# Kernel tuning notes

Hardware: AMD Instinct MI355X
Metric: run time of the kernel (lower is better)

Reference implementation:

```python
import jax, jax.numpy as jnp
import numpy as np

T, B, DIN, H, AA, L = 1024, 32, 256, 256, 21, 2


def setup_inputs() -> dict:
    key = jax.random.key(0)
    ks = jax.random.split(key, 8)
    scale = 0.05

    def rn(i, shape):
        return jax.random.normal(ks[i], shape, dtype=jnp.float32) * scale

    return {
        "x": jax.random.normal(ks[0], (B, T, DIN), dtype=jnp.float32),
        "hidden": jnp.zeros((2 * L, B, H), jnp.float32),  # accepted but unused, as in torch forward
        # layer 0: input DIN -> per-direction 4 chunks of H; layer 1: input 2H
        "w_l0": rn(1, (DIN, 2, 4, H)),
        "wc_l0": rn(2, (2, 2, H)),            # [dir, (v_f, v_r), H]
        "b_l0": jnp.zeros((2, 2, H), jnp.float32),  # [dir, (b_f, b_r), H]
        "w_l1": rn(3, (2 * H, 2, 4, H)),
        "wc_l1": rn(4, (2, 2, H)),
        "b_l1": jnp.zeros((2, 2, H), jnp.float32),
        "fc1_w": rn(5, (H, 2 * H)),
        "fc1_b": jnp.zeros((H,), jnp.float32),
        "lp_w": rn(6, (AA, H)),
        "lp_b": jnp.zeros((AA,), jnp.float32),
    }


def _sru_scan(u, vf, vr, bf, br):
    # u: (T, B, 4, H) with chunks [candidate, forget, reset, highway]
    def step(c, ut):
        f = jax.nn.sigmoid(ut[:, 1] + vf * c + bf)
        c2 = f * c + (1.0 - f) * ut[:, 0]
        r = jax.nn.sigmoid(ut[:, 2] + vr * c + br)
        h = r * c2 + (1.0 - r) * ut[:, 3]
        return c2, h

    c0 = jnp.zeros((u.shape[1], u.shape[-1]), u.dtype)
    _, hs = jax.lax.scan(step, c0, u)
    return hs  # (T, B, H)


def _sru_layer(x, w, wc, b):
    # x: (T, B, Din); w: (Din, 2, 4, H)
    U = jnp.einsum('tbd,dnkh->tbnkh', x, w)
    hf = _sru_scan(U[:, :, 0], wc[0, 0], wc[0, 1], b[0, 0], b[0, 1])
    hb = _sru_scan(U[::-1, :, 1], wc[1, 0], wc[1, 1], b[1, 0], b[1, 1])[::-1]
    return jnp.concatenate([hf, hb], axis=-1)  # (T, B, 2H)


def reference(x, hidden, w_l0, wc_l0, b_l0, w_l1, wc_l1, b_l1, fc1_w, fc1_b, lp_w, lp_b):
    h = jnp.transpose(x, (1, 0, 2))  # (T, B, DIN)
    h = _sru_layer(h, w_l0, wc_l0, b_l0)
    h = _sru_layer(h, w_l1, wc_l1, b_l1)
    h = jnp.transpose(h, (1, 0, 2))  # (B, T, 2H)
    h = h @ fc1_w.T + fc1_b
    logits = h @ lp_w.T + lp_b
    return jax.nn.log_softmax(logits, axis=-1)  # (B, T, AA)
```

## Files before the change

kernel.cpp:

```cpp
#include <hip/hip_runtime.h>
#include <hip/hip_bf16.h>

#define T_DIM 1024
#define B_DIM 32
#define DIN_DIM 256
#define H_DIM 256
#define AA_DIM 21
#define M_ROWS (B_DIM * T_DIM)

typedef __attribute__((ext_vector_type(8))) short bf16x8;
typedef __attribute__((ext_vector_type(4))) float f32x4;

typedef __attribute__((address_space(3))) void lds_void;
typedef const __attribute__((address_space(1))) void glb_void;

#define LOG2E_F 1.44269504088896340736f

__device__ __forceinline__ void gload_lds16(const void* g, void* l) {
    __builtin_amdgcn_global_load_lds((glb_void*)g, (lds_void*)l, 16, 0, 0);
}

__device__ __forceinline__ float b2f(unsigned short v) {
    unsigned u = ((unsigned)v) << 16;
    float f;
    __builtin_memcpy(&f, &u, 4);
    return f;
}

__device__ __forceinline__ unsigned short f2bu(float f) {
    __hip_bfloat16 h = __float2bfloat16(f);
    unsigned short u;
    __builtin_memcpy(&u, &h, 2);
    return u;
}

#define CVT_V0 2097152
#define CVT_N1 524288
#define CVT_N2 1048576
#define CVT_V3 32768
#define CVT_N4 8192
#define CVT_TOT (CVT_V0 + CVT_N1 + CVT_N2 + CVT_V3 + CVT_N4)
__global__ __launch_bounds__(256) void cvt_all(
    const float* __restrict__ x,  const float* __restrict__ w0,
    const float* __restrict__ w1, const float* __restrict__ fcw,
    const float* __restrict__ lpw,
    __hip_bfloat16* __restrict__ xb,  __hip_bfloat16* __restrict__ w0t,
    __hip_bfloat16* __restrict__ w1t, __hip_bfloat16* __restrict__ fcwb,
    __hip_bfloat16* __restrict__ lpwb)
{
    int i = blockIdx.x * 256 + threadIdx.x;
    if (i < CVT_V0) {
        float4 v = ((const float4*)x)[i];
        ushort4 o = { f2bu(v.x), f2bu(v.y), f2bu(v.z), f2bu(v.w) };
        ((ushort4*)xb)[i] = o;
        return;
    }
    i -= CVT_V0;
    if (i < CVT_N1) {
        int kk = i >> 11, rem = i & 2047;
        int dir = rem >> 10, k = (rem >> 8) & 3, h = rem & 255;
        w0t[(long)(dir * 1024 + h * 4 + k) * 256 + kk] = __float2bfloat16(w0[i]);
        return;
    }
    i -= CVT_N1;
    if (i < CVT_N2) {
        int kk = i >> 11, rem = i & 2047;
        int dir = rem >> 10, k = (rem >> 8) & 3, h = rem & 255;
        w1t[(long)(dir * 1024 + h * 4 + k) * 512 + kk] = __float2bfloat16(w1[i]);
        return;
    }
    i -= CVT_N2;
    if (i < CVT_V3) {
        float4 v = ((const float4*)fcw)[i];
        ushort4 o = { f2bu(v.x), f2bu(v.y), f2bu(v.z), f2bu(v.w) };
        ((ushort4*)fcwb)[i] = o;
        return;
    }
    i -= CVT_V3;
    if (i < CVT_N4) {
        int n = i >> 8, k = i & 255;
        lpwb[i] = __float2bfloat16(n < AA_DIM ? lpw[n * 256 + k] : 0.0f);
    }
}

__device__ __forceinline__ void stage_tile256(
    const __hip_bfloat16* __restrict__ A,
    const __hip_bfloat16* __restrict__ Bt,
    char* buf, long m0, long n0, int K, int kb,
    int wave, int ldrow, int gkoff)
{
#pragma unroll
    for (int i = 0; i < 4; ++i) {
        const int cid = wave * 4 + i;
        const int rc  = cid >> 1;
        const int kh  = cid & 1;
        const long row = rc * 16 + ldrow;
        const int koff = kb + kh * 32 + gkoff;
        gload_lds16(A  + (m0 + row) * (long)K + koff,
                    buf + rc * 2048 + kh * 1024);
        gload_lds16(Bt + (n0 + row) * (long)K + koff,
                    buf + 32768 + rc * 2048 + kh * 1024);
    }
}

#define MFMA16(d, a, b) d = __builtin_amdgcn_mfma_f32_16x16x32_bf16(a, b, d, 0, 0, 0)

__global__ __launch_bounds__(512, 2) void gemm256_u2(
    const __hip_bfloat16* __restrict__ A,
    const __hip_bfloat16* __restrict__ Bt,
    __hip_bfloat16* __restrict__ C,
    int K, int nbShift)
{
    __shared__ __align__(16) char smb[131072];

    const int tid  = threadIdx.x;
    const int lane = tid & 63;
    const int wave = tid >> 6;
    const int wm   = wave >> 2;
    const int wn   = wave & 3;

    const int L  = blockIdx.x;
    const int s  = L >> 3;
    const int nb = s & ((1 << nbShift) - 1);
    const int mb = ((s >> nbShift) << 3) + (L & 7);
    const long n0 = (long)nb * 256;
    const long m0 = (long)mb * 256;

    const int ldrow = lane >> 2;
    const int ldq   = lane & 3;
    const int gq    = ldq ^ ((ldrow >> 1) & 3);
    const int gkoff = gq * 8;

    const int fr = lane & 15;
    const int kq = lane >> 4;
    const int sw = (kq ^ ((fr >> 1) & 3)) * 16;

    f32x4 acc[8][4] = {};
    const int NT = K >> 6;

    stage_tile256(A, Bt, smb,         m0, n0, K, 0,  wave, ldrow, gkoff);
    __builtin_amdgcn_sched_barrier(0);
    stage_tile256(A, Bt, smb + 65536, m0, n0, K, 64, wave, ldrow, gkoff);
    asm volatile("s_waitcnt vmcnt(8)" ::: "memory");
    __builtin_amdgcn_s_barrier();

    for (int kt = 0; kt < NT; ++kt) {
        char* rb = smb + (kt & 1) * 65536;
        const char* Ab = rb + (wm * 8) * 2048;
        const char* Bb = rb + 32768 + (wn * 4) * 2048;
        bf16x8 a0[4], a1[4], bv[4];

#pragma unroll
        for (int i = 0; i < 4; ++i) {
            a0[i] = *(const bf16x8*)(Ab + i * 2048 + fr * 64 + sw);
            bv[i] = *(const bf16x8*)(Bb + i * 2048 + fr * 64 + sw);
        }
        __builtin_amdgcn_s_barrier();
        __builtin_amdgcn_s_setprio(1);
#pragma unroll
        for (int i = 0; i < 4; ++i)
#pragma unroll
            for (int j = 0; j < 4; ++j)
                MFMA16(acc[i][j], a0[i], bv[j]);
        __builtin_amdgcn_s_setprio(0);
        __builtin_amdgcn_s_barrier();

#pragma unroll
        for (int i = 0; i < 4; ++i)
            a1[i] = *(const bf16x8*)(Ab + (4 + i) * 2048 + fr * 64 + sw);
        __builtin_amdgcn_s_barrier();
        __builtin_amdgcn_s_setprio(1);
#pragma unroll
        for (int i = 0; i < 4; ++i)
#pragma unroll
            for (int j = 0; j < 4; ++j)
                MFMA16(acc[4 + i][j], a1[i], bv[j]);
        __builtin_amdgcn_s_setprio(0);
        __builtin_amdgcn_s_barrier();

#pragma unroll
        for (int i = 0; i < 4; ++i) {
            a0[i] = *(const bf16x8*)(Ab + i * 2048 + 1024 + fr * 64 + sw);
            bv[i] = *(const bf16x8*)(Bb + i * 2048 + 1024 + fr * 64 + sw);
        }
        __builtin_amdgcn_s_barrier();
        __builtin_amdgcn_s_setprio(1);
#pragma unroll
        for (int i = 0; i < 4; ++i)
#pragma unroll
            for (int j = 0; j < 4; ++j)
                MFMA16(acc[i][j], a0[i], bv[j]);
        __builtin_amdgcn_s_setprio(0);
        __builtin_amdgcn_s_barrier();

#pragma unroll
        for (int i = 0; i < 4; ++i)
            a1[i] = *(const bf16x8*)(Ab + (4 + i) * 2048 + 1024 + fr * 64 + sw);
        __builtin_amdgcn_s_barrier();
        __builtin_amdgcn_s_setprio(1);
#pragma unroll
        for (int i = 0; i < 4; ++i)
#pragma unroll
            for (int j = 0; j < 4; ++j)
                MFMA16(acc[4 + i][j], a1[i], bv[j]);
        __builtin_amdgcn_s_setprio(0);
        __builtin_amdgcn_s_barrier();

        __builtin_amdgcn_sched_barrier(0);
        if (kt + 2 < NT) {
            stage_tile256(A, Bt, rb, m0, n0, K, (kt + 2) * 64,
                          wave, ldrow, gkoff);
            asm volatile("s_waitcnt vmcnt(8)" ::: "memory");
        } else if (kt + 1 < NT) {
            asm volatile("s_waitcnt vmcnt(0)" ::: "memory");
        }
        __builtin_amdgcn_s_barrier();
    }

    const int col_l = lane & 15;
    const int row_l = (lane >> 4) * 4;
    __hip_bfloat16* smC = (__hip_bfloat16*)smb;
    const int chunk = tid & 31;
    const int rbase = tid >> 5;
#pragma unroll
    for (int p = 0; p < 2; ++p) {
        __syncthreads();
        if (wm == p) {
#pragma unroll
            for (int i = 0; i < 8; ++i)
#pragma unroll
                for (int j = 0; j < 4; ++j)
#pragma unroll
                    for (int r = 0; r < 4; ++r)
                        smC[(i * 16 + row_l + r) * 264 + wn * 64 + j * 16 + col_l] =
                            __float2bfloat16(acc[i][j][r]);
        }
        __syncthreads();
#pragma unroll
        for (int it = 0; it < 8; ++it) {
            const int rr = it * 16 + rbase;
            bf16x8 v = *(const bf16x8*)(smC + rr * 264 + chunk * 8);
            const long gr  = m0 + p * 128 + rr;
            const long gc0 = n0 + chunk * 8;
            const int bI  = (int)(gr >> 10);
            const int t   = (int)(gr & 1023);
            const int dir = (int)(gc0 >> 10);
            const int hg  = ((int)gc0 >> 8) & 3;
            const int beta = bI * 8 + dir * 4 + hg;
            const long base = ((long)beta * 1024 + t) * 256 + ((int)gc0 & 255);
            *(bf16x8*)(C + base) = v;
        }
    }
}

template<int U2OUT>
__global__ __launch_bounds__(256) void gemm_bf16(
    const __hip_bfloat16* __restrict__ A,
    const __hip_bfloat16* __restrict__ Bt,
    const float* __restrict__ bias,
    __hip_bfloat16* __restrict__ C,
    int M, int N, int K, int nbShift)
{
    __shared__ __align__(16) char smb[32768];

    const int tid  = threadIdx.x;
    const int lane = tid & 63;
    const int wave = tid >> 6;
    const int wm = wave & 1;
    const int wn = wave >> 1;

    const int L   = blockIdx.x;
    const int s   = L >> 3;
    const int nb  = s & ((1 << nbShift) - 1);
    const int mb  = ((s >> nbShift) << 3) + (L & 7);
    const long n0 = (long)nb * 128;
    const long m0 = (long)mb * 128;

    f32x4 acc[4][4] = {};

    const int ldrow = lane >> 2;
    const int ldq   = lane & 3;
    const int gq    = ldq ^ ((ldrow >> 1) & 3);
    const int gkoff = gq * 8;

    const int fr = lane & 15;
    const int kq = lane >> 4;
    const int sw = (kq ^ ((fr >> 1) & 3)) * 16;

    for (int kb = 0; kb < K; kb += 64) {
        __syncthreads();
#pragma unroll
        for (int i = 0; i < 4; ++i) {
            const int cid = wave * 4 + i;
            const int rc  = cid >> 1;
            const int kh  = cid & 1;
            const long row = rc * 16 + ldrow;
            const int koff = kb + kh * 32 + gkoff;
            gload_lds16(A  + (m0 + row) * (long)K + koff,
                        smb + rc * 2048 + kh * 1024);
            gload_lds16(Bt + (n0 + row) * (long)K + koff,
                        smb + 16384 + rc * 2048 + kh * 1024);
        }
        __syncthreads();

#pragma unroll
        for (int ss = 0; ss < 2; ++ss) {
            bf16x8 af[4], bfv[4];
#pragma unroll
            for (int i = 0; i < 4; ++i) {
                af[i]  = *(const bf16x8*)(smb + (wm * 4 + i) * 2048 + ss * 1024 + fr * 64 + sw);
                bfv[i] = *(const bf16x8*)(smb + 16384 + (wn * 4 + i) * 2048 + ss * 1024 + fr * 64 + sw);
            }
#pragma unroll
            for (int i = 0; i < 4; ++i)
#pragma unroll
                for (int j = 0; j < 4; ++j)
                    acc[i][j] = __builtin_amdgcn_mfma_f32_16x16x32_bf16(
                        af[i], bfv[j], acc[i][j], 0, 0, 0);
        }
    }

    const int col_l = lane & 15;
    const int row_l = (lane >> 4) * 4;
    __hip_bfloat16* smC = (__hip_bfloat16*)smb;
#pragma unroll
    for (int p = 0; p < 2; ++p) {
        __syncthreads();
        if (wm == p) {
#pragma unroll
            for (int j = 0; j < 4; ++j) {
                const long gc = n0 + wn * 64 + j * 16 + col_l;
                const float bv = bias ? bias[gc] : 0.0f;
#pragma unroll
                for (int i = 0; i < 4; ++i)
#pragma unroll
                    for (int r = 0; r < 4; ++r)
                        smC[(i * 16 + row_l + r) * 132 + wn * 64 + j * 16 + col_l] =
                            __float2bfloat16(acc[i][j][r] + bv);
            }
        }
        __syncthreads();
        const int cb = (tid & 7) * 16;
#pragma unroll
        for (int s2 = 0; s2 < 2; ++s2) {
            const int rr = s2 * 32 + (tid >> 3);
            const long gr = m0 + p * 64 + rr;
            bf16x8 v0 = *(const bf16x8*)(smC + rr * 132 + cb);
            bf16x8 v1 = *(const bf16x8*)(smC + rr * 132 + cb + 8);
            if (U2OUT) {
                const int bI  = (int)(gr >> 10);
                const int t   = (int)(gr & 1023);
                const long gc0 = n0 + cb;
                const int dir = (int)(gc0 >> 10);
                const int hg  = ((int)gc0 >> 8) & 3;
                const int beta = bI * 8 + dir * 4 + hg;
                const long base = ((long)beta * 1024 + t) * 256 + (gc0 & 255);
                *(bf16x8*)(C + base)     = v0;
                *(bf16x8*)(C + base + 8) = v1;
            } else {
                *(bf16x8*)(C + gr * (long)N + n0 + cb)     = v0;
                *(bf16x8*)(C + gr * (long)N + n0 + cb + 8) = v1;
            }
        }
    }
}

#define SCAN_S 64
#define SCAN_NB (T_DIM / SCAN_S)
#define GRP 16

__device__ __forceinline__ float scan_step(
    uint2 u, float c, float nvf, float nvr, float nbf, float nbr,
    __hip_bfloat16* hq)
{
    float u0, u1, u2, u3;
    unsigned a0 = u.x << 16, a1 = u.x & 0xffff0000u;
    unsigned a2 = u.y << 16, a3 = u.y & 0xffff0000u;
    __builtin_memcpy(&u0, &a0, 4); __builtin_memcpy(&u1, &a1, 4);
    __builtin_memcpy(&u2, &a2, 4); __builtin_memcpy(&u3, &a3, 4);
    const float nf0 = __builtin_fmaf(-LOG2E_F, u1, nbf);
    const float nr0 = __builtin_fmaf(-LOG2E_F, u2, nbr);
    const float ef = __builtin_amdgcn_exp2f(__builtin_fmaf(nvf, c, nf0));
    const float er = __builtin_amdgcn_exp2f(__builtin_fmaf(nvr, c, nr0));
    const float f  = __builtin_amdgcn_rcpf(1.0f + ef);
    const float r  = __builtin_amdgcn_rcpf(1.0f + er);
    const float c2 = __builtin_fmaf(f, c - u0, u0);
    const float hv = __builtin_fmaf(r, c2 - u3, u3);
    *hq = __float2bfloat16(hv);
    return c2;
}

__global__ __launch_bounds__(256) void sru_scan(
    const __hip_bfloat16* __restrict__ U2,
    const float* __restrict__ wc,
    const float* __restrict__ bias,
    __hip_bfloat16* __restrict__ hout)
{
    __shared__ __align__(16) char lds[2 * SCAN_S * 512];
    const int tid  = threadIdx.x;
    const int wave = tid >> 6;
    const int lane = tid & 63;
    const int beta = blockIdx.x;
    const int b    = beta >> 3;
    const int dir  = (beta >> 2) & 1;
    const int hg   = beta & 3;
    const int h    = hg * 64 + lane;

    const char* gslice = (const char*)U2 + (size_t)beta * (1024 * 512);

    const float nvf = -LOG2E_F * wc[(dir * 2 + 0) * H_DIM + h];
    const float nvr = -LOG2E_F * wc[(dir * 2 + 1) * H_DIM + h];
    const float nbf = -LOG2E_F * bias[(dir * 2 + 0) * H_DIM + h];
    const float nbr = -LOG2E_F * bias[(dir * 2 + 1) * H_DIM + h];
    __hip_bfloat16* hp = hout + ((long)(b * 1024 + (dir ? 1023 : 0))) * 512 + dir * 256 + h;
    const long hstep = dir ? -512L : 512L;
    float c = 0.0f;

    const int plane = lane & 31;

    if (wave > 0) {
        for (int p = wave - 1; p < SCAN_S / 2; p += 3) {
            const int sl = 2 * p + (lane >> 5);
            const int t  = dir ? (1023 - sl) : sl;
            gload_lds16(gslice + (size_t)t * 512 + plane * 16, lds + p * 1024);
        }
    }
    __syncthreads();

    for (int bat = 0; bat < SCAN_NB; ++bat) {
        if (wave > 0) {
            if (bat + 1 < SCAN_NB) {
                char* halfN = lds + ((bat + 1) & 1) * (SCAN_S * 512);
                const int tb = (bat + 1) * SCAN_S;
                for (int p = wave - 1; p < SCAN_S / 2; p += 3) {
                    const int sl = tb + 2 * p + (lane >> 5);
                    const int t  = dir ? (1023 - sl) : sl;
                    gload_lds16(gslice + (size_t)t * 512 + plane * 16,
                                halfN + p * 1024);
                }
            }
        } else {
            const char* half = lds + (bat & 1) * (SCAN_S * 512);
            __hip_bfloat16* hq = hp + (long)(bat * SCAN_S) * hstep;
            uint2 qa[GRP], qb[GRP];
#pragma unroll
            for (int j = 0; j < GRP; ++j)
                qa[j] = *(const uint2*)(half + (0 * GRP + j) * 512 + (lane << 3));
#pragma unroll
            for (int j = 0; j < GRP; ++j)
                qb[j] = *(const uint2*)(half + (1 * GRP + j) * 512 + (lane << 3));
#pragma unroll
            for (int j = 0; j < GRP; ++j)
                c = scan_step(qa[j], c, nvf, nvr, nbf, nbr, hq + (long)j * hstep);
#pragma unroll
            for (int j = 0; j < GRP; ++j)
                qa[j] = *(const uint2*)(half + (2 * GRP + j) * 512 + (lane << 3));
#pragma unroll
            for (int j = 0; j < GRP; ++j)
                c = scan_step(qb[j], c, nvf, nvr, nbf, nbr, hq + (long)(GRP + j) * hstep);
#pragma unroll
            for (int j = 0; j < GRP; ++j)
                qb[j] = *(const uint2*)(half + (3 * GRP + j) * 512 + (lane << 3));
#pragma unroll
            for (int j = 0; j < GRP; ++j)
                c = scan_step(qa[j], c, nvf, nvr, nbf, nbr, hq + (long)(2 * GRP + j) * hstep);
#pragma unroll
            for (int j = 0; j < GRP; ++j)
                c = scan_step(qb[j], c, nvf, nvr, nbf, nbr, hq + (long)(3 * GRP + j) * hstep);
        }
        __syncthreads();
    }
}

__global__ __launch_bounds__(256) void logits_mfma(
    const __hip_bfloat16* __restrict__ fc,
    const __hip_bfloat16* __restrict__ lpwb,
    const float* __restrict__ lpb,
    float* __restrict__ out)
{
    __shared__ __align__(16) char smb[25088];
    const int tid  = threadIdx.x;
    const int lane = tid & 63;
    const int wave = tid >> 6;
    const long m0  = (long)blockIdx.x * 128;

    for (int idx = tid; idx < 32 * 32; idx += 256) {
        const int rw = idx >> 5, sl = idx & 31;
        *(bf16x8*)(smb + rw * 528 + sl * 16) =
            *(const bf16x8*)(lpwb + rw * 256 + sl * 8);
    }

    const int ldrow = lane >> 2;
    const int ldq   = lane & 3;
    const int gq    = ldq ^ ((ldrow >> 1) & 3);
    const int gkoff = gq * 8;

    const int fr = lane & 15;
    const int kq = lane >> 4;
    const int sw = (kq ^ ((fr >> 1) & 3)) * 16;

    f32x4 acc[2][2] = {};
    for (int kc = 0; kc < 8; ++kc) {
        __syncthreads();
#pragma unroll
        for (int i = 0; i < 2; ++i) {
            const int rc = wave * 2 + i;
            gload_lds16(fc + (m0 + rc * 16 + ldrow) * 256 + kc * 32 + gkoff,
                        smb + 16896 + rc * 1024);
        }
        __syncthreads();
        bf16x8 af[2], bfv[2];
#pragma unroll
        for (int i = 0; i < 2; ++i)
            af[i] = *(const bf16x8*)(smb + 16896 + (wave * 2 + i) * 1024 + fr * 64 + sw);
#pragma unroll
        for (int j = 0; j < 2; ++j)
            bfv[j] = *(const bf16x8*)(smb + (j * 16 + fr) * 528 + kc * 64 + kq * 16);
#pragma unroll
        for (int i = 0; i < 2; ++i)
#pragma unroll
            for (int j = 0; j < 2; ++j)
                acc[i][j] = __builtin_amdgcn_mfma_f32_16x16x32_bf16(
                    af[i], bfv[j], acc[i][j], 0, 0, 0);
    }

    __syncthreads();
    float* smC = (float*)smb;
    const int col_l = lane & 15;
    const int row_l = (lane >> 4) * 4;
#pragma unroll
    for (int j = 0; j < 2; ++j) {
        const int gc = j * 16 + col_l;
        const float bv = (gc < AA_DIM) ? lpb[gc] : 0.0f;
#pragma unroll
        for (int i = 0; i < 2; ++i)
#pragma unroll
            for (int r = 0; r < 4; ++r)
                smC[(wave * 32 + i * 16 + row_l + r) * 36 + gc] = acc[i][j][r] + bv;
    }
    __syncthreads();
    if (tid < 128) {
        const float* rowp = smC + tid * 36;
        float m = rowp[0];
#pragma unroll
        for (int a = 1; a < AA_DIM; ++a) m = fmaxf(m, rowp[a]);
        float s = 0.0f;
#pragma unroll
        for (int a = 0; a < AA_DIM; ++a) s += __expf(rowp[a] - m);
        const float lse = __logf(s) + m;
        float* op = out + (m0 + tid) * AA_DIM;
#pragma unroll
        for (int a = 0; a < AA_DIM; ++a) op[a] = rowp[a] - lse;
    }
}

extern "C" void kernel_launch(void* const* d_in, const int* in_sizes, int n_in,
                              void* d_out, int out_size, void* d_ws, size_t ws_size,
                              hipStream_t stream)
{
    const float* x     = (const float*)d_in[0];
    const float* w_l0  = (const float*)d_in[2];
    const float* wc_l0 = (const float*)d_in[3];
    const float* b_l0  = (const float*)d_in[4];
    const float* w_l1  = (const float*)d_in[5];
    const float* wc_l1 = (const float*)d_in[6];
    const float* b_l1  = (const float*)d_in[7];
    const float* fc1_w = (const float*)d_in[8];
    const float* fc1_b = (const float*)d_in[9];
    const float* lp_w  = (const float*)d_in[10];
    const float* lp_b  = (const float*)d_in[11];
    float* out = (float*)d_out;

    char* ws = (char*)d_ws;
    __hip_bfloat16* U      = (__hip_bfloat16*)(ws);
    __hip_bfloat16* h0b    = (__hip_bfloat16*)(ws + 134217728);
    __hip_bfloat16* h1b    = (__hip_bfloat16*)(ws + 167772160);
    __hip_bfloat16* xb     = (__hip_bfloat16*)(ws + 201326592);
    __hip_bfloat16* fcob   = xb;
    __hip_bfloat16* w0t    = (__hip_bfloat16*)(ws + 218103808);
    __hip_bfloat16* w1t    = (__hip_bfloat16*)(ws + 219152384);
    __hip_bfloat16* fc1wb  = (__hip_bfloat16*)(ws + 221249536);
    __hip_bfloat16* lpwb   = (__hip_bfloat16*)(ws + 221511680);

    cvt_all<<<(CVT_TOT + 255) / 256, 256, 0, stream>>>(
        x, w_l0, w_l1, fc1_w, lp_w, xb, w0t, w1t, fc1wb, lpwb);

    gemm256_u2<<<1024, 512, 0, stream>>>(xb, w0t, U, DIN_DIM, 3);
    sru_scan<<<256, 256, 0, stream>>>(U, wc_l0, b_l0, h0b);
    gemm256_u2<<<1024, 512, 0, stream>>>(h0b, w1t, U, 512, 3);
    sru_scan<<<256, 256, 0, stream>>>(U, wc_l1, b_l1, h1b);
    gemm_bf16<0><<<512, 256, 0, stream>>>(
        h1b, fc1wb, fc1_b, fcob, M_ROWS, 256, 512, 1);
    logits_mfma<<<M_ROWS / 128, 256, 0, stream>>>(fcob, lpwb, lp_b, out);
}
```

Measured before the change: 389.1 us.

## Fuse fc1 GEMM with logits projection and log-softmax in one kernel

Replaces the separate fc1 GEMM and logits kernels with one fused kernel. Each 512-thread block computes a 128x256 fc1 tile with double-buffered LDS staging, keeps the bf16 result in LDS, and then runs the 21-class projection and log-softmax on it. This removes the global write and re-read of the fc1 intermediate and one kernel launch. In exchange, only 256 blocks at one block per CU run, each loading the full N=256 weight slice, so latency hiding may suffer.

```diff
diff --git a/kernel.cpp b/kernel.cpp
--- a/kernel.cpp
+++ b/kernel.cpp
@@ -18,13 +18,6 @@
 
 __device__ __forceinline__ void gload_lds16(const void* g, void* l) {
     __builtin_amdgcn_global_load_lds((glb_void*)g, (lds_void*)l, 16, 0, 0);
-}
-
-__device__ __forceinline__ float b2f(unsigned short v) {
-    unsigned u = ((unsigned)v) << 16;
-    float f;
-    __builtin_memcpy(&f, &u, 4);
-    return f;
 }
 
 __device__ __forceinline__ unsigned short f2bu(float f) {
@@ -83,6 +76,8 @@
     }
 }
 
+#define MFMA16(d, a, b) d = __builtin_amdgcn_mfma_f32_16x16x32_bf16(a, b, d, 0, 0, 0)
+
 __device__ __forceinline__ void stage_tile256(
     const __hip_bfloat16* __restrict__ A,
     const __hip_bfloat16* __restrict__ Bt,
@@ -102,8 +97,6 @@
                     buf + 32768 + rc * 2048 + kh * 1024);
     }
 }
-
-#define MFMA16(d, a, b) d = __builtin_amdgcn_mfma_f32_16x16x32_bf16(a, b, d, 0, 0, 0)
 
 __global__ __launch_bounds__(512, 2) void gemm256_u2(
     const __hip_bfloat16* __restrict__ A,
@@ -249,118 +242,6 @@
             const int beta = bI * 8 + dir * 4 + hg;
             const long base = ((long)beta * 1024 + t) * 256 + ((int)gc0 & 255);
             *(bf16x8*)(C + base) = v;
-        }
-    }
-}
-
-template<int U2OUT>
-__global__ __launch_bounds__(256) void gemm_bf16(
-    const __hip_bfloat16* __restrict__ A,
-    const __hip_bfloat16* __restrict__ Bt,
-    const float* __restrict__ bias,
-    __hip_bfloat16* __restrict__ C,
-    int M, int N, int K, int nbShift)
-{
-    __shared__ __align__(16) char smb[32768];
-
-    const int tid  = threadIdx.x;
-    const int lane = tid & 63;
-    const int wave = tid >> 6;
-    const int wm = wave & 1;
-    const int wn = wave >> 1;
-
-    const int L   = blockIdx.x;
-    const int s   = L >> 3;
-    const int nb  = s & ((1 << nbShift) - 1);
-    const int mb  = ((s >> nbShift) << 3) + (L & 7);
-    const long n0 = (long)nb * 128;
-    const long m0 = (long)mb * 128;
-
-    f32x4 acc[4][4] = {};
-
-    const int ldrow = lane >> 2;
-    const int ldq   = lane & 3;
-    const int gq    = ldq ^ ((ldrow >> 1) & 3);
-    const int gkoff = gq * 8;
-
-    const int fr = lane & 15;
-    const int kq = lane >> 4;
-    const int sw = (kq ^ ((fr >> 1) & 3)) * 16;
-
-    for (int kb = 0; kb < K; kb += 64) {
-        __syncthreads();
-#pragma unroll
-        for (int i = 0; i < 4; ++i) {
-            const int cid = wave * 4 + i;
-            const int rc  = cid >> 1;
-            const int kh  = cid & 1;
-            const long row = rc * 16 + ldrow;
-            const int koff = kb + kh * 32 + gkoff;
-            gload_lds16(A  + (m0 + row) * (long)K + koff,
-                        smb + rc * 2048 + kh * 1024);
-            gload_lds16(Bt + (n0 + row) * (long)K + koff,
-                        smb + 16384 + rc * 2048 + kh * 1024);
-        }
-        __syncthreads();
-
-#pragma unroll
-        for (int ss = 0; ss < 2; ++ss) {
-            bf16x8 af[4], bfv[4];
-#pragma unroll
-            for (int i = 0; i < 4; ++i) {
-                af[i]  = *(const bf16x8*)(smb + (wm * 4 + i) * 2048 + ss * 1024 + fr * 64 + sw);
-                bfv[i] = *(const bf16x8*)(smb + 16384 + (wn * 4 + i) * 2048 + ss * 1024 + fr * 64 + sw);
-            }
-#pragma unroll
-            for (int i = 0; i < 4; ++i)
-#pragma unroll
-                for (int j = 0; j < 4; ++j)
-                    acc[i][j] = __builtin_amdgcn_mfma_f32_16x16x32_bf16(
-                        af[i], bfv[j], acc[i][j], 0, 0, 0);
-        }
-    }
-
-    const int col_l = lane & 15;
-    const int row_l = (lane >> 4) * 4;
-    __hip_bfloat16* smC = (__hip_bfloat16*)smb;
-#pragma unroll
-    for (int p = 0; p < 2; ++p) {
-        __syncthreads();
-        if (wm == p) {
-#pragma unroll
-            for (int j = 0; j < 4; ++j) {
-                const long gc = n0 + wn * 64 + j * 16 + col_l;
-                const float bv = bias ? bias[gc] : 0.0f;
-#pragma unroll
-                for (int i = 0; i < 4; ++i)
-#pragma unroll
-                    for (int r = 0; r < 4; ++r)
-                        smC[(i * 16 + row_l + r) * 132 + wn * 64 + j * 16 + col_l] =
-                            __float2bfloat16(acc[i][j][r] + bv);
-            }
-        }
-        __syncthreads();
-        const int cb = (tid & 7) * 16;
-#pragma unroll
-        for (int s2 = 0; s2 < 2; ++s2) {
-            const int rr = s2 * 32 + (tid >> 3);
-            const long gr = m0 + p * 64 + rr;
-            bf16x8 v0 = *(const bf16x8*)(smC + rr * 132 + cb);
-            bf16x8 v1 = *(const bf16x8*)(smC + rr * 132 + cb + 8);
-            if (U2OUT) {
-                const int bI  = (int)(gr >> 10);
-                const int t   = (int)(gr & 1023);
-                const long gc0 = n0 + cb;
-                const int dir = (int)(gc0 >> 10);
-                const int hg  = ((int)gc0 >> 8) & 3;
-                const int beta = bI * 8 + dir * 4 + hg;
-                const long base = ((long)beta * 1024 + t) * 256 + (gc0 & 255);
-                *(bf16x8*)(C + base)     = v0;
-                *(bf16x8*)(C + base + 8) = v1;
-            } else {
-                *(bf16x8*)(C + gr * (long)N + n0 + cb)     = v0;
-                *(bf16x8*)(C + gr * (long)N + n0 + cb + 8) = v1;
-            }
         }
     }
 }
@@ -472,23 +353,26 @@
     }
 }
 
-__global__ __launch_bounds__(256) void logits_mfma(
-    const __hip_bfloat16* __restrict__ fc,
+#define FL_BUF 49152
+#define FL_LP  98304
+#define FL_SCR 115200
+#define FL_TOT 133632
+
+__global__ __launch_bounds__(512, 1) void fc_logits(
+    const __hip_bfloat16* __restrict__ A,
+    const __hip_bfloat16* __restrict__ Bw,
+    const float* __restrict__ fcb,
     const __hip_bfloat16* __restrict__ lpwb,
     const float* __restrict__ lpb,
     float* __restrict__ out)
 {
-    __shared__ __align__(16) char smb[25088];
+    __shared__ __align__(16) char lds[FL_TOT];
     const int tid  = threadIdx.x;
     const int lane = tid & 63;
     const int wave = tid >> 6;
+    const int wm   = wave & 1;
+    const int wn   = wave >> 1;
     const long m0  = (long)blockIdx.x * 128;
-
-    for (int idx = tid; idx < 32 * 32; idx += 256) {
-        const int rw = idx >> 5, sl = idx & 31;
-        *(bf16x8*)(smb + rw * 528 + sl * 16) =
-            *(const bf16x8*)(lpwb + rw * 256 + sl * 8);
-    }
 
     const int ldrow = lane >> 2;
     const int ldq   = lane & 3;
@@ -499,48 +383,109 @@
     const int kq = lane >> 4;
     const int sw = (kq ^ ((fr >> 1) & 3)) * 16;
 
-    f32x4 acc[2][2] = {};
-    for (int kc = 0; kc < 8; ++kc) {
-        __syncthreads();
-#pragma unroll
-        for (int i = 0; i < 2; ++i) {
-            const int rc = wave * 2 + i;
-            gload_lds16(fc + (m0 + rc * 16 + ldrow) * 256 + kc * 32 + gkoff,
-                        smb + 16896 + rc * 1024);
-        }
-        __syncthreads();
-        bf16x8 af[2], bfv[2];
-#pragma unroll
-        for (int i = 0; i < 2; ++i)
-            af[i] = *(const bf16x8*)(smb + 16896 + (wave * 2 + i) * 1024 + fr * 64 + sw);
-#pragma unroll
-        for (int j = 0; j < 2; ++j)
-            bfv[j] = *(const bf16x8*)(smb + (j * 16 + fr) * 528 + kc * 64 + kq * 16);
-#pragma unroll
-        for (int i = 0; i < 2; ++i)
-#pragma unroll
-            for (int j = 0; j < 2; ++j)
-                acc[i][j] = __builtin_amdgcn_mfma_f32_16x16x32_bf16(
-                    af[i], bfv[j], acc[i][j], 0, 0, 0);
-    }
-
-    __syncthreads();
-    float* smC = (float*)smb;
+    for (int idx = tid; idx < 1024; idx += 512) {
+        const int rw = idx >> 5, sl = idx & 31;
+        *(bf16x8*)(lds + FL_LP + rw * 528 + sl * 16) =
+            *(const bf16x8*)(lpwb + rw * 256 + sl * 8);
+    }
+    __builtin_amdgcn_sched_barrier(0);
+
+    f32x4 acc[4][4] = {};
+
+#define STAGE_FL(BUF, KB)                                                   \
+    do {                                                                    \
+        _Pragma("unroll")                                                   \
+        for (int i2 = 0; i2 < 6; ++i2) {                                    \
+            const int sg = wave * 6 + i2;                        \
+            if (sg < 16) {                              \
+                const int rc = sg >> 1, kh = sg & 1;                        \
+                gload_lds16(A + (m0 + rc * 16 + ldrow) * 512L +             \
+                                (KB) + kh * 32 + gkoff,                     \
+                            (BUF) + rc * 2048 + kh * 1024);                 \
+            } else {                                   \
+                const int t2 = sg - 16, rc = t2 >> 1, kh = t2 & 1;          \
+                gload_lds16(Bw + (rc * 16 + ldrow) * 512L +                 \
+                                 (KB) + kh * 32 + gkoff,                    \
+                            (BUF) + 16384 + rc * 2048 + kh * 1024);         \
+            }                                                               \
+        }                                                                   \
+    } while (0)
+
+    STAGE_FL(lds, 0);
+
+    for (int kt = 0; kt < 8; ++kt) {
+        char* cur = lds + (kt & 1) * FL_BUF;
+        char* nxt = lds + ((kt + 1) & 1) * FL_BUF;
+        __builtin_amdgcn_sched_barrier(0);
+        if (kt + 1 < 8) {
+            STAGE_FL(nxt, (kt + 1) * 64);
+            __builtin_amdgcn_sched_barrier(0);
+            asm volatile("s_waitcnt vmcnt(6)" ::: "memory");
+        } else {
+            asm volatile("s_waitcnt vmcnt(0)" ::: "memory");
+        }
+        __builtin_amdgcn_s_barrier();
+
+#pragma unroll
+        for (int ss = 0; ss < 2; ++ss) {
+            bf16x8 af[4], bfv[4];
+#pragma unroll
+            for (int i = 0; i < 4; ++i) {
+                af[i]  = *(const bf16x8*)(cur + (wm * 4 + i) * 2048 + ss * 1024 + fr * 64 + sw);
+                bfv[i] = *(const bf16x8*)(cur + 16384 + (wn * 4 + i) * 2048 + ss * 1024 + fr * 64 + sw);
+            }
+            __builtin_amdgcn_s_setprio(1);
+#pragma unroll
+            for (int i = 0; i < 4; ++i)
+#pragma unroll
+                for (int j = 0; j < 4; ++j)
+                    MFMA16(acc[i][j], af[i], bfv[j]);
+            __builtin_amdgcn_s_setprio(0);
+        }
+        __builtin_amdgcn_s_barrier();
+    }
+#undef STAGE_FL
+
     const int col_l = lane & 15;
     const int row_l = (lane >> 4) * 4;
+    __hip_bfloat16* fcX = (__hip_bfloat16*)lds;
+#pragma unroll
+    for (int j = 0; j < 4; ++j) {
+        const int gc = wn * 64 + j * 16 + col_l;
+        const float bv = fcb[gc];
+#pragma unroll
+        for (int i = 0; i < 4; ++i)
+#pragma unroll
+            for (int r = 0; r < 4; ++r)
+                fcX[(wm * 64 + i * 16 + row_l + r) * 260 + gc] =
+                    __float2bfloat16(acc[i][j][r] + bv);
+    }
+    __syncthreads();
+
+    const int rb = wave * 16;
+    f32x4 acc2[2] = {};
+#pragma unroll
+    for (int kc = 0; kc < 8; ++kc) {
+        bf16x8 afx = *(const bf16x8*)(lds + (rb + fr) * 520 + kc * 64 + kq * 16);
+        bf16x8 b0  = *(const bf16x8*)(lds + FL_LP + fr * 528 + kc * 64 + kq * 16);
+        bf16x8 b1  = *(const bf16x8*)(lds + FL_LP + (16 + fr) * 528 + kc * 64 + kq * 16);
+        MFMA16(acc2[0], afx, b0);
+        MFMA16(acc2[1], afx, b1);
+    }
+
+    float* smL = (float*)(lds + FL_SCR);
 #pragma unroll
     for (int j = 0; j < 2; ++j) {
         const int gc = j * 16 + col_l;
         const float bv = (gc < AA_DIM) ? lpb[gc] : 0.0f;
 #pragma unroll
-        for (int i = 0; i < 2; ++i)
-#pragma unroll
-            for (int r = 0; r < 4; ++r)
-                smC[(wave * 32 + i * 16 + row_l + r) * 36 + gc] = acc[i][j][r] + bv;
+        for (int r = 0; r < 4; ++r)
+            smL[(rb + row_l + r) * 36 + gc] = acc2[j][r] + bv;
     }
     __syncthreads();
+
     if (tid < 128) {
-        const float* rowp = smC + tid * 36;
+        const float* rowp = smL + tid * 36;
         float m = rowp[0];
 #pragma unroll
         for (int a = 1; a < AA_DIM; ++a) m = fmaxf(m, rowp[a]);
@@ -576,7 +521,6 @@
     __hip_bfloat16* h0b    = (__hip_bfloat16*)(ws + 134217728);
     __hip_bfloat16* h1b    = (__hip_bfloat16*)(ws + 167772160);
     __hip_bfloat16* xb     = (__hip_bfloat16*)(ws + 201326592);
-    __hip_bfloat16* fcob   = xb;
     __hip_bfloat16* w0t    = (__hip_bfloat16*)(ws + 218103808);
     __hip_bfloat16* w1t    = (__hip_bfloat16*)(ws + 219152384);
     __hip_bfloat16* fc1wb  = (__hip_bfloat16*)(ws + 221249536);
@@ -589,7 +533,6 @@
     sru_scan<<<256, 256, 0, stream>>>(U, wc_l0, b_l0, h0b);
     gemm256_u2<<<1024, 512, 0, stream>>>(h0b, w1t, U, 512, 3);
     sru_scan<<<256, 256, 0, stream>>>(U, wc_l1, b_l1, h1b);
-    gemm_bf16<0><<<512, 256, 0, stream>>>(
-        h1b, fc1wb, fc1_b, fcob, M_ROWS, 256, 512, 1);
-    logits_mfma<<<M_ROWS / 128, 256, 0, stream>>>(fcob, lpwb, lp_b, out);
-}
+
+    fc_logits<<<256, 512, 0, stream>>>(h1b, fc1wb, fc1_b, lpwb, lp_b, out);
+}
```

After: 378.7 us (median of 4 runs). 1.03x faster.
